# Kernel optimization log

Hardware: AMD Instinct MI355X
Metric: run time of the kernel (lower is better)

Reference implementation:

```python
import jax, jax.numpy as jnp
import numpy as np

LN_EPS = 1e-5  # torch.nn.LayerNorm default


def setup_inputs() -> dict:
    key = jax.random.key(0)
    ks = jax.random.split(key, 6)
    b, e, c, h, w, m = 4, 16, 256, 32, 64, 1024
    return {
        "x": jax.random.normal(ks[0], (b, e, c, h, w), dtype=jnp.float32),
        "ln_w": jnp.ones((c, h, w), dtype=jnp.float32),
        "ln_b": jnp.zeros((c, h, w), dtype=jnp.float32),
        "w_in": jax.random.normal(ks[1], (c, m), dtype=jnp.float32) * (1.0 / np.sqrt(c)),
        "b_in": jax.random.normal(ks[2], (m,), dtype=jnp.float32) * 0.01,
        "w_out": jax.random.normal(ks[3], (m, c), dtype=jnp.float32) * (1.0 / np.sqrt(m)),
        "b_out": jax.random.normal(ks[4], (c,), dtype=jnp.float32) * 0.01,
        "gamma": jnp.full((c,), 1e-6, dtype=jnp.float32),
    }


def reference(x, ln_w, ln_b, w_in, b_in, w_out, b_out, gamma):
    # LayerNorm over the last 3 dims (c, h, w) with affine params of shape (c, h, w)
    mu = jnp.mean(x, axis=(-3, -2, -1), keepdims=True)
    var = jnp.var(x, axis=(-3, -2, -1), keepdims=True)  # biased, matches torch
    y = (x - mu) * jax.lax.rsqrt(var + LN_EPS)
    y = y * ln_w + ln_b  # broadcast (c,h,w) over (b,e,...)

    # b e c h w -> b e h w c
    y = jnp.moveaxis(y, 2, -1)
    t = jax.nn.gelu(y @ w_in + b_in, approximate=False)  # torch GELU is exact erf
    t = (t @ w_out + b_out) * gamma  # layer scale on channel dim

    # b e h w c -> b e c h w, residual add
    return x + jnp.moveaxis(t, -1, 2)
```

## Files before the change

### kernel.cpp

```cpp
#include <hip/hip_runtime.h>
#include <math.h>

#define NS 64
#define CD 256
#define HW 2048
#define MD 1024
#define SAMPLE (CD * HW)
#define LN_EPS 1e-5f

#define PB 128
#define MC 32
#define NCH (MD / MC)

typedef float f32x4 __attribute__((ext_vector_type(4)));
typedef long i64;

__device__ __forceinline__ int swz(int p) {
  int k = (p ^ (p >> 2)) & 15;
  return ((k & 7) << 4) | (k & 8);
}

__device__ __forceinline__ void gl_lds16(const unsigned char* g, unsigned char* l) {
  __builtin_amdgcn_global_load_lds(
      (const __attribute__((address_space(1))) unsigned char*)g,
      (__attribute__((address_space(3))) unsigned char*)l, 16, 0, 0);
}

__global__ __launch_bounds__(256) void k_prep(const float* __restrict__ w_in,
                                              const float* __restrict__ w_out,
                                              unsigned char* __restrict__ w_in8p,
                                              unsigned char* __restrict__ w_out8p) {
  int id = blockIdx.x * 256 + threadIdx.x;
  if (id < 65536) {
    int i = id;
    int f = i >> 7, l = (i >> 1) & 63, j0 = (i & 1) * 4;
    int m = (f >> 3) * 16 + (l & 15);
    int c0 = (f & 7) * 32 + (l >> 4) * 8 + j0;
    float a = w_in[(size_t)(c0 + 0) * MD + m];
    float b = w_in[(size_t)(c0 + 1) * MD + m];
    float c = w_in[(size_t)(c0 + 2) * MD + m];
    float d = w_in[(size_t)(c0 + 3) * MD + m];
    int r = __builtin_amdgcn_cvt_pk_fp8_f32(a, b, 0, false);
    r = __builtin_amdgcn_cvt_pk_fp8_f32(c, d, r, true);
    ((int*)w_in8p)[i] = r;
  } else {
    int i = id - 65536;
    int g = i >> 7, l = (i >> 1) & 63, j0 = (i & 1) * 4;
    int c = (g & 15) * 16 + (l & 15);
    int m0 = (g >> 4) * 32 + (l >> 4) * 8 + j0;
    float a = w_out[(size_t)(m0 + 0) * CD + c];
    float b = w_out[(size_t)(m0 + 1) * CD + c];
    float cc = w_out[(size_t)(m0 + 2) * CD + c];
    float d = w_out[(size_t)(m0 + 3) * CD + c];
    int r = __builtin_amdgcn_cvt_pk_fp8_f32(a, b, 0, false);
    r = __builtin_amdgcn_cvt_pk_fp8_f32(cc, d, r, true);
    ((int*)w_out8p)[i] = r;
  }
}

__global__ __launch_bounds__(256) void k_stats1(const float* __restrict__ x,
                                                double* __restrict__ partial) {
  int s = blockIdx.x >> 3, sl = blockIdx.x & 7;
  const float4* p = (const float4*)(x + (size_t)s * SAMPLE + (size_t)sl * 65536);
  double sum = 0.0, ssq = 0.0;
  for (int i = 0; i < 64; ++i) {
    float4 v = p[i * 256 + threadIdx.x];
    sum += (double)v.x + (double)v.y + (double)v.z + (double)v.w;
    ssq += (double)v.x * v.x + (double)v.y * v.y + (double)v.z * v.z + (double)v.w * v.w;
  }
  for (int off = 32; off; off >>= 1) {
    sum += __shfl_down(sum, off);
    ssq += __shfl_down(ssq, off);
  }
  __shared__ double red[4][2];
  int wv = threadIdx.x >> 6, ln = threadIdx.x & 63;
  if (ln == 0) { red[wv][0] = sum; red[wv][1] = ssq; }
  __syncthreads();
  if (threadIdx.x == 0) {
    for (int i = 1; i < 4; ++i) { sum += red[i][0]; ssq += red[i][1]; }
    partial[blockIdx.x * 2] = sum;
    partial[blockIdx.x * 2 + 1] = ssq;
  }
}

__global__ void k_stats2(const double* __restrict__ partial, float* __restrict__ stats) {
  int s = threadIdx.x;
  double sum = 0.0, ssq = 0.0;
  for (int i = 0; i < 8; ++i) {
    sum += partial[(s * 8 + i) * 2];
    ssq += partial[(s * 8 + i) * 2 + 1];
  }
  double mean = sum / (double)SAMPLE;
  double var = ssq / (double)SAMPLE - mean * mean;
  stats[s * 2] = (float)mean;
  stats[s * 2 + 1] = (float)(1.0 / sqrt(var + (double)LN_EPS));
}

__global__ __launch_bounds__(512, 4) void k_fused(
    const float* __restrict__ x, const float* __restrict__ ln_w, const float* __restrict__ ln_b,
    const float* __restrict__ b_in, const float* __restrict__ b_out, const float* __restrict__ gamma,
    const unsigned char* __restrict__ w_in8p, const unsigned char* __restrict__ w_out8p,
    const float* __restrict__ stats, float* __restrict__ out) {
  extern __shared__ unsigned char smem[];
  unsigned char* Ysh = smem;
  unsigned char* Wsh1 = smem + 32768;
  unsigned char* Wsh2 = smem + 49152;

  const int tid = threadIdx.x;
  const int lane = tid & 63, l15 = lane & 15, l4 = lane >> 4;
  const int wv = tid >> 6;
  const int s = blockIdx.x >> 4;
  const int p0 = (blockIdx.x & 15) * PB;
  const float mu = stats[s * 2], rstd = stats[s * 2 + 1];
  const float a_ln = rstd, c_ln = -mu * rstd;
  const size_t xbase = (size_t)s * SAMPLE;

  gl_lds16(w_in8p + wv * 1024 + lane * 16, Wsh1 + wv * 1024);
  gl_lds16(w_out8p + wv * 1024 + lane * 16, Wsh2 + wv * 1024);

  #pragma unroll
  for (int it = 0; it < 4; ++it) {
    int bid = it * 512 + tid;
    int c0 = (bid >> 5) * 4, pp = (bid & 31) * 4;
    float yv[4][4];
    #pragma unroll
    for (int i = 0; i < 4; ++i) {
      size_t off = (size_t)(c0 + i) * HW + p0 + pp;
      float4 xv = *(const float4*)(x + xbase + off);
      float4 lw = *(const float4*)(ln_w + off);
      float4 lb = *(const float4*)(ln_b + off);
      yv[i][0] = fmaf(fmaf(xv.x, a_ln, c_ln), lw.x, lb.x);
      yv[i][1] = fmaf(fmaf(xv.y, a_ln, c_ln), lw.y, lb.y);
      yv[i][2] = fmaf(fmaf(xv.z, a_ln, c_ln), lw.z, lb.z);
      yv[i][3] = fmaf(fmaf(xv.w, a_ln, c_ln), lw.w, lb.w);
    }
    #pragma unroll
    for (int j = 0; j < 4; ++j) {
      int p = pp + j;
      int r = __builtin_amdgcn_cvt_pk_fp8_f32(yv[0][j], yv[1][j], 0, false);
      r = __builtin_amdgcn_cvt_pk_fp8_f32(yv[2][j], yv[3][j], r, true);
      *(int*)&Ysh[p * 256 + (c0 ^ swz(p))] = r;
    }
  }

  const int strip = wv * 16;
  const int pY = strip + l15;
  const int sY = swz(pY);
  f32x4 acc2[16] = {};

  __syncthreads();

  i64 breg[8];
  #pragma unroll
  for (int kk = 0; kk < 8; ++kk)
    breg[kk] = *(const i64*)&Ysh[pY * 256 + ((kk * 32 + l4 * 8) ^ sY)];

  i64 a2_prev = 0;

  for (int ch = 0; ch < NCH; ++ch) {
    if (ch) __syncthreads();

    if (ch + 1 < NCH) {
      const size_t co = (size_t)(ch + 1) * 8192;
      gl_lds16(w_in8p + co + wv * 1024 + lane * 16,
               Wsh1 + ((ch + 1) & 1) * 8192 + wv * 1024);
      gl_lds16(w_out8p + co + wv * 1024 + lane * 16,
               Wsh2 + ((ch + 1) % 3) * 8192 + wv * 1024);
    }

    __builtin_amdgcn_s_setprio(1);
    if (ch) {
      const unsigned char* W2 = Wsh2 + ((ch - 1) % 3) * 8192;
      #pragma unroll
      for (int ct = 0; ct < 16; ++ct) {
        i64 b2 = *(const i64*)&W2[ct * 512 + lane * 8];
        acc2[ct] = __builtin_amdgcn_mfma_f32_16x16x32_fp8_fp8(a2_prev, b2, acc2[ct], 0, 0, 0);
      }
    }

    const unsigned char* W1 = Wsh1 + (ch & 1) * 8192;
    f32x4 acc1[2] = {};
    #pragma unroll
    for (int kk = 0; kk < 8; ++kk) {
      i64 a0 = *(const i64*)&W1[(kk)*512 + lane * 8];
      i64 a1 = *(const i64*)&W1[(8 + kk) * 512 + lane * 8];
      acc1[0] = __builtin_amdgcn_mfma_f32_16x16x32_fp8_fp8(a0, breg[kk], acc1[0], 0, 0, 0);
      acc1[1] = __builtin_amdgcn_mfma_f32_16x16x32_fp8_fp8(a1, breg[kk], acc1[1], 0, 0, 0);
    }
    __builtin_amdgcn_s_setprio(0);

    int pk0, pk1;
    #pragma unroll
    for (int mt = 0; mt < 2; ++mt) {
      const float4 bi = *(const float4*)&b_in[ch * 32 + mt * 16 + l4 * 4];
      float g[4];
      #pragma unroll
      for (int r = 0; r < 4; ++r) {
        float t = acc1[mt][r] + ((const float*)&bi)[r];
        g[r] = t * __builtin_amdgcn_rcpf(1.0f + __expf(-1.702f * t));
      }
      int pk = __builtin_amdgcn_cvt_pk_fp8_f32(g[0], g[1], 0, false);
      pk = __builtin_amdgcn_cvt_pk_fp8_f32(g[2], g[3], pk, true);
      if (mt == 0) pk0 = pk; else pk1 = pk;
    }

    {
      const int sl = l15 + 32 * (l4 & 1);
      int v0a = __shfl(pk0, sl), v0b = __shfl(pk1, sl);
      int v1a = __shfl(pk0, sl + 16), v1b = __shfl(pk1, sl + 16);
      int vlo = (l4 & 2) ? v0b : v0a;
      int vhi = (l4 & 2) ? v1b : v1a;
      a2_prev = (i64)((((unsigned long long)(unsigned)vhi) << 32) | (unsigned)vlo);
    }
  }

  {
    const unsigned char* W2 = Wsh2 + ((NCH - 1) % 3) * 8192;
    #pragma unroll
    for (int ct = 0; ct < 16; ++ct) {
      i64 b2 = *(const i64*)&W2[ct * 512 + lane * 8];
      acc2[ct] = __builtin_amdgcn_mfma_f32_16x16x32_fp8_fp8(a2_prev, b2, acc2[ct], 0, 0, 0);
    }
  }

  #pragma unroll
  for (int ct = 0; ct < 16; ++ct) {
    int cc = ct * 16 + l15;
    float gm = gamma[cc], bo = b_out[cc];
    int p = p0 + strip + l4 * 4;
    size_t off = xbase + (size_t)cc * HW + p;
    float4 xv = *(const float4*)(x + off);
    float4 o;
    #pragma unroll
    for (int r = 0; r < 4; ++r)
      ((float*)&o)[r] = ((const float*)&xv)[r] + gm * (acc2[ct][r] + bo);
    *(float4*)(out + off) = o;
  }
}

extern "C" void kernel_launch(void* const* d_in, const int* in_sizes, int n_in,
                              void* d_out, int out_size, void* d_ws, size_t ws_size,
                              hipStream_t stream) {
  const float* x = (const float*)d_in[0];
  const float* ln_w = (const float*)d_in[1];
  const float* ln_b = (const float*)d_in[2];
  const float* w_in = (const float*)d_in[3];
  const float* b_in = (const float*)d_in[4];
  const float* w_out = (const float*)d_in[5];
  const float* b_out = (const float*)d_in[6];
  const float* gamma = (const float*)d_in[7];
  float* out = (float*)d_out;

  char* ws = (char*)d_ws;
  unsigned char* w_in8p = (unsigned char*)ws;
  unsigned char* w_out8p = (unsigned char*)(ws + 262144);
  double* partial = (double*)(ws + 524288);
  float* stats = (float*)(ws + 524288 + 8192);

  k_prep<<<512, 256, 0, stream>>>(w_in, w_out, w_in8p, w_out8p);
  k_stats1<<<512, 256, 0, stream>>>(x, partial);
  k_stats2<<<1, 64, 0, stream>>>(partial, stats);

  const int lds_bytes = 32768 + 16384 + 24576;
  hipFuncSetAttribute((const void*)k_fused, hipFuncAttributeMaxDynamicSharedMemorySize,
                      lds_bytes);
  k_fused<<<1024, 512, lds_bytes, stream>>>(x, ln_w, ln_b, b_in, b_out, gamma,
                                            w_in8p, w_out8p, stats, out);
}
```

Baseline: 182.9 us.

## Double hidden-dim chunk to 64 and repack weights and LDS to match

Widens each hidden-dimension chunk from 32 to 64 columns, so the fused loop runs half as many iterations, barriers and prefetch rounds. The fp8 weight packing kernel and the LDS buffer layout are changed to match. The Y tile is placed so it overlaps the later W_out ring buffers, which is safe only because of a barrier added after Y is read into registers. In exchange, more accumulator registers and a larger LDS footprint (80 KB per block) may limit occupancy.

```diff
diff --git a/kernel.cpp b/kernel.cpp
--- a/kernel.cpp
+++ b/kernel.cpp
@@ -9,7 +9,7 @@
 #define LN_EPS 1e-5f
 
 #define PB 128
-#define MC 32
+#define MC 64
 #define NCH (MD / MC)
 
 typedef float f32x4 __attribute__((ext_vector_type(4)));
@@ -33,9 +33,10 @@
   int id = blockIdx.x * 256 + threadIdx.x;
   if (id < 65536) {
     int i = id;
-    int f = i >> 7, l = (i >> 1) & 63, j0 = (i & 1) * 4;
-    int m = (f >> 3) * 16 + (l & 15);
-    int c0 = (f & 7) * 32 + (l >> 4) * 8 + j0;
+    int g2 = i >> 7, l = (i >> 1) & 63, j0 = (i & 1) * 4;
+    int ch = g2 >> 5, mt = (g2 >> 3) & 3, kk = g2 & 7;
+    int m = ch * 64 + mt * 16 + (l & 15);
+    int c0 = kk * 32 + (l >> 4) * 8 + j0;
     float a = w_in[(size_t)(c0 + 0) * MD + m];
     float b = w_in[(size_t)(c0 + 1) * MD + m];
     float c = w_in[(size_t)(c0 + 2) * MD + m];
@@ -46,8 +47,9 @@
   } else {
     int i = id - 65536;
     int g = i >> 7, l = (i >> 1) & 63, j0 = (i & 1) * 4;
-    int c = (g & 15) * 16 + (l & 15);
-    int m0 = (g >> 4) * 32 + (l >> 4) * 8 + j0;
+    int ch = g >> 5, ct = (g >> 1) & 15, ks = g & 1;
+    int c = ct * 16 + (l & 15);
+    int m0 = ch * 64 + ks * 32 + (l >> 4) * 8 + j0;
     float a = w_out[(size_t)(m0 + 0) * CD + c];
     float b = w_out[(size_t)(m0 + 1) * CD + c];
     float cc = w_out[(size_t)(m0 + 2) * CD + c];
@@ -102,9 +104,7 @@
     const unsigned char* __restrict__ w_in8p, const unsigned char* __restrict__ w_out8p,
     const float* __restrict__ stats, float* __restrict__ out) {
   extern __shared__ unsigned char smem[];
-  unsigned char* Ysh = smem;
-  unsigned char* Wsh1 = smem + 32768;
-  unsigned char* Wsh2 = smem + 49152;
+  unsigned char* Ysh = smem + 16384;
 
   const int tid = threadIdx.x;
   const int lane = tid & 63, l15 = lane & 15, l4 = lane >> 4;
@@ -115,8 +115,10 @@
   const float a_ln = rstd, c_ln = -mu * rstd;
   const size_t xbase = (size_t)s * SAMPLE;
 
-  gl_lds16(w_in8p + wv * 1024 + lane * 16, Wsh1 + wv * 1024);
-  gl_lds16(w_out8p + wv * 1024 + lane * 16, Wsh2 + wv * 1024);
+  gl_lds16(w_in8p + wv * 2048 + lane * 16, smem + 49152 + wv * 2048);
+  gl_lds16(w_in8p + wv * 2048 + 1024 + lane * 16, smem + 49152 + wv * 2048 + 1024);
+  gl_lds16(w_out8p + wv * 2048 + lane * 16, smem + wv * 2048);
+  gl_lds16(w_out8p + wv * 2048 + 1024 + lane * 16, smem + wv * 2048 + 1024);
 
   #pragma unroll
   for (int it = 0; it < 4; ++it) {
@@ -155,71 +157,82 @@
   for (int kk = 0; kk < 8; ++kk)
     breg[kk] = *(const i64*)&Ysh[pY * 256 + ((kk * 32 + l4 * 8) ^ sY)];
 
-  i64 a2_prev = 0;
+  __syncthreads();
+
+  i64 a2p0 = 0, a2p1 = 0;
 
   for (int ch = 0; ch < NCH; ++ch) {
     if (ch) __syncthreads();
 
     if (ch + 1 < NCH) {
-      const size_t co = (size_t)(ch + 1) * 8192;
-      gl_lds16(w_in8p + co + wv * 1024 + lane * 16,
-               Wsh1 + ((ch + 1) & 1) * 8192 + wv * 1024);
-      gl_lds16(w_out8p + co + wv * 1024 + lane * 16,
-               Wsh2 + ((ch + 1) % 3) * 8192 + wv * 1024);
+      const size_t co = (size_t)(ch + 1) * 16384;
+      unsigned char* d1 = smem + 49152 + ((ch + 1) & 1) * 16384;
+      unsigned char* d2 = smem + ((ch + 1) % 3) * 16384;
+      gl_lds16(w_in8p + co + wv * 2048 + lane * 16, d1 + wv * 2048);
+      gl_lds16(w_in8p + co + wv * 2048 + 1024 + lane * 16, d1 + wv * 2048 + 1024);
+      gl_lds16(w_out8p + co + wv * 2048 + lane * 16, d2 + wv * 2048);
+      gl_lds16(w_out8p + co + wv * 2048 + 1024 + lane * 16, d2 + wv * 2048 + 1024);
     }
 
     __builtin_amdgcn_s_setprio(1);
     if (ch) {
-      const unsigned char* W2 = Wsh2 + ((ch - 1) % 3) * 8192;
+      const unsigned char* W2 = smem + ((ch - 1) % 3) * 16384;
       #pragma unroll
       for (int ct = 0; ct < 16; ++ct) {
-        i64 b2 = *(const i64*)&W2[ct * 512 + lane * 8];
-        acc2[ct] = __builtin_amdgcn_mfma_f32_16x16x32_fp8_fp8(a2_prev, b2, acc2[ct], 0, 0, 0);
+        i64 b20 = *(const i64*)&W2[(ct * 2) * 512 + lane * 8];
+        i64 b21 = *(const i64*)&W2[(ct * 2 + 1) * 512 + lane * 8];
+        acc2[ct] = __builtin_amdgcn_mfma_f32_16x16x32_fp8_fp8(a2p0, b20, acc2[ct], 0, 0, 0);
+        acc2[ct] = __builtin_amdgcn_mfma_f32_16x16x32_fp8_fp8(a2p1, b21, acc2[ct], 0, 0, 0);
       }
     }
 
-    const unsigned char* W1 = Wsh1 + (ch & 1) * 8192;
-    f32x4 acc1[2] = {};
+    const unsigned char* W1 = smem + 49152 + (ch & 1) * 16384;
+    f32x4 acc1[4] = {};
     #pragma unroll
     for (int kk = 0; kk < 8; ++kk) {
-      i64 a0 = *(const i64*)&W1[(kk)*512 + lane * 8];
-      i64 a1 = *(const i64*)&W1[(8 + kk) * 512 + lane * 8];
-      acc1[0] = __builtin_amdgcn_mfma_f32_16x16x32_fp8_fp8(a0, breg[kk], acc1[0], 0, 0, 0);
-      acc1[1] = __builtin_amdgcn_mfma_f32_16x16x32_fp8_fp8(a1, breg[kk], acc1[1], 0, 0, 0);
+      #pragma unroll
+      for (int mt = 0; mt < 4; ++mt) {
+        i64 a = *(const i64*)&W1[(mt * 8 + kk) * 512 + lane * 8];
+        acc1[mt] = __builtin_amdgcn_mfma_f32_16x16x32_fp8_fp8(a, breg[kk], acc1[mt], 0, 0, 0);
+      }
     }
     __builtin_amdgcn_s_setprio(0);
 
-    int pk0, pk1;
-    #pragma unroll
-    for (int mt = 0; mt < 2; ++mt) {
-      const float4 bi = *(const float4*)&b_in[ch * 32 + mt * 16 + l4 * 4];
-      float g[4];
+    #pragma unroll
+    for (int h = 0; h < 2; ++h) {
+      int pk0, pk1;
       #pragma unroll
-      for (int r = 0; r < 4; ++r) {
-        float t = acc1[mt][r] + ((const float*)&bi)[r];
-        g[r] = t * __builtin_amdgcn_rcpf(1.0f + __expf(-1.702f * t));
+      for (int mtl = 0; mtl < 2; ++mtl) {
+        const float4 bi = *(const float4*)&b_in[ch * 64 + h * 32 + mtl * 16 + l4 * 4];
+        const f32x4 A = acc1[h * 2 + mtl];
+        float g[4];
+        #pragma unroll
+        for (int r = 0; r < 4; ++r) {
+          float t = A[r] + ((const float*)&bi)[r];
+          g[r] = t * __builtin_amdgcn_rcpf(1.0f + __expf(-1.702f * t));
+        }
+        int pk = __builtin_amdgcn_cvt_pk_fp8_f32(g[0], g[1], 0, false);
+        pk = __builtin_amdgcn_cvt_pk_fp8_f32(g[2], g[3], pk, true);
+        if (mtl == 0) pk0 = pk; else pk1 = pk;
       }
-      int pk = __builtin_amdgcn_cvt_pk_fp8_f32(g[0], g[1], 0, false);
-      pk = __builtin_amdgcn_cvt_pk_fp8_f32(g[2], g[3], pk, true);
-      if (mt == 0) pk0 = pk; else pk1 = pk;
-    }
-
-    {
       const int sl = l15 + 32 * (l4 & 1);
       int v0a = __shfl(pk0, sl), v0b = __shfl(pk1, sl);
       int v1a = __shfl(pk0, sl + 16), v1b = __shfl(pk1, sl + 16);
       int vlo = (l4 & 2) ? v0b : v0a;
       int vhi = (l4 & 2) ? v1b : v1a;
-      a2_prev = (i64)((((unsigned long long)(unsigned)vhi) << 32) | (unsigned)vlo);
+      i64 a2n = (i64)((((unsigned long long)(unsigned)vhi) << 32) | (unsigned)vlo);
+      if (h == 0) a2p0 = a2n; else a2p1 = a2n;
     }
   }
 
   {
-    const unsigned char* W2 = Wsh2 + ((NCH - 1) % 3) * 8192;
+    const unsigned char* W2 = smem + ((NCH - 1) % 3) * 16384;
     #pragma unroll
     for (int ct = 0; ct < 16; ++ct) {
-      i64 b2 = *(const i64*)&W2[ct * 512 + lane * 8];
-      acc2[ct] = __builtin_amdgcn_mfma_f32_16x16x32_fp8_fp8(a2_prev, b2, acc2[ct], 0, 0, 0);
+      i64 b20 = *(const i64*)&W2[(ct * 2) * 512 + lane * 8];
+      i64 b21 = *(const i64*)&W2[(ct * 2 + 1) * 512 + lane * 8];
+      acc2[ct] = __builtin_amdgcn_mfma_f32_16x16x32_fp8_fp8(a2p0, b20, acc2[ct], 0, 0, 0);
+      acc2[ct] = __builtin_amdgcn_mfma_f32_16x16x32_fp8_fp8(a2p1, b21, acc2[ct], 0, 0, 0);
     }
   }
 
@@ -261,7 +274,7 @@
   k_stats1<<<512, 256, 0, stream>>>(x, partial);
   k_stats2<<<1, 64, 0, stream>>>(partial, stats);
 
-  const int lds_bytes = 32768 + 16384 + 24576;
+  const int lds_bytes = 81920;
   hipFuncSetAttribute((const void*)k_fused, hipFuncAttributeMaxDynamicSharedMemorySize,
                       lds_bytes);
   k_fused<<<1024, 512, lds_bytes, stream>>>(x, ln_w, ln_b, b_in, b_out, gamma,
```

After: 191.4 us. 1.05x slower.
